# Performance work log

Hardware: AMD Instinct MI355X
Metric: run time of the kernel (lower is better)

Reference implementation:

```python
import jax, jax.numpy as jnp
import numpy as np

EPS_GN = 1e-5
EPS_ATTN = 1e-6
HEADS = 4
DIM_HEAD = 32
GROUPS = 32  # min(32, channels=128)


def group_norm(x, weight, bias, groups=GROUPS, eps=EPS_GN):
    # x: [b, c, h, w]
    b, c, h, w = x.shape
    xg = x.reshape(b, groups, c // groups, h, w)
    mean = xg.mean(axis=(2, 3, 4), keepdims=True)
    var = xg.var(axis=(2, 3, 4), keepdims=True)
    xg = (xg - mean) * jax.lax.rsqrt(var + eps)
    x = xg.reshape(b, c, h, w)
    return x * weight[None, :, None, None] + bias[None, :, None, None]


def conv1x1(x, w):
    # x: [b, c, h, w], w: [out, in] -> [b, out, h, w]
    return jnp.einsum('bchw,oc->bohw', x, w)


def setup_inputs() -> dict:
    key = jax.random.key(0)
    ks = jax.random.split(key, 6)
    b, c, h, w = 16, 128, 128, 128
    inner = HEADS * DIM_HEAD  # 128
    x = jax.random.normal(ks[0], (b, c, h, w), dtype=jnp.float32)
    gn1_w = jnp.ones((c,), jnp.float32) + 0.02 * jax.random.normal(ks[1], (c,), jnp.float32)
    gn1_b = 0.02 * jax.random.normal(ks[2], (c,), jnp.float32)
    w_qkv = jax.random.normal(ks[3], (inner * 3, c), jnp.float32) / np.sqrt(c)
    w_out = jax.random.normal(ks[4], (c, inner), jnp.float32) / np.sqrt(inner)
    gn2_w = jnp.ones((c,), jnp.float32) + 0.02 * jax.random.normal(ks[5], (c,), jnp.float32)
    gn2_b = jnp.zeros((c,), jnp.float32)
    return {"x": x, "gn1_w": gn1_w, "gn1_b": gn1_b, "w_qkv": w_qkv,
            "w_out": w_out, "gn2_w": gn2_w, "gn2_b": gn2_b}


def reference(x, gn1_w, gn1_b, w_qkv, w_out, gn2_w, gn2_b):
    b, c, h, w = x.shape
    residual = x
    xn = group_norm(x, gn1_w, gn1_b)
    qkv = conv1x1(xn, w_qkv)                      # [b, 3*inner, h, w]
    q, k, v = jnp.split(qkv, 3, axis=1)
    # 'b (heads d) h w -> b heads (h w) d'
    def to_tokens(t):
        return t.reshape(b, HEADS, DIM_HEAD, h * w).transpose(0, 1, 3, 2)
    q, k, v = to_tokens(q), to_tokens(k), to_tokens(v)
    q = jax.nn.elu(q) + 1.0
    k = jax.nn.elu(k) + 1.0
    k_sum = k.sum(axis=2)                          # [b, heads, d]
    kv = jnp.einsum('bhnd,bhne->bhde', k, v)       # [b, heads, d, d]
    qk_sum = jnp.einsum('bhnd,bhd->bhn', q, k_sum) # [b, heads, n]
    qkv_out = jnp.einsum('bhnd,bhde->bhne', q, kv) # [b, heads, n, d]
    out = qkv_out / (qk_sum[..., None] + EPS_ATTN)
    # 'b heads (h w) d -> b (heads d) h w'
    out = out.transpose(0, 1, 3, 2).reshape(b, HEADS * DIM_HEAD, h, w)
    out = conv1x1(out, w_out)
    out = group_norm(out, gn2_w, gn2_b)
    return out + residual
```

## Files before the change

kernel.cpp:

```cpp
#include <hip/hip_runtime.h>

#define B_   16
#define C_   128
#define HW_  16384

typedef __attribute__((ext_vector_type(4))) float  floatx4;
typedef __attribute__((ext_vector_type(8))) short  short8;
typedef __attribute__((ext_vector_type(4))) short  short4v;

static __device__ __forceinline__ unsigned short f2bf(float f){
  unsigned int u = __float_as_uint(f);
  u += 0x7FFFu + ((u >> 16) & 1u);
  return (unsigned short)(u >> 16);
}
static __device__ __forceinline__ float bf2f(unsigned short h){
  return __uint_as_float(((unsigned int)h) << 16);
}
static __device__ __forceinline__ float elu1(float v){
  return v > 0.f ? v + 1.f : __expf(v);
}
static __device__ __forceinline__ int keyx(int n){ return ((n >> 1) & 7) ^ ((n >> 4) & 7); }

__global__ __launch_bounds__(512) void k_xprep(const float* __restrict__ x,
    unsigned short* __restrict__ xT, float* __restrict__ gn1part){
  int blk = blockIdx.x;
  int b = blk >> 6, tile = blk & 63;
  int n0 = tile * 256;
  __shared__ unsigned short XS[32768];
  int t = threadIdx.x, w = t >> 6, l = t & 63;
  float sk[4], sk2[4];
  #pragma unroll
  for (int k = 0; k < 4; ++k){ sk[k] = 0.f; sk2[k] = 0.f; }
  #pragma unroll
  for (int k = 0; k < 4; ++k){
    float4 f4[4];
    #pragma unroll
    for (int j = 0; j < 4; ++j){
      int c = 16*w + 4*k + j;
      f4[j] = *(const float4*)(x + ((size_t)(b*128 + c))*HW_ + n0 + 4*l);
    }
    #pragma unroll
    for (int j = 0; j < 4; ++j){
      sk[k]  += f4[j].x + f4[j].y + f4[j].z + f4[j].w;
      sk2[k] += f4[j].x*f4[j].x + f4[j].y*f4[j].y + f4[j].z*f4[j].z + f4[j].w*f4[j].w;
    }
    int c0 = 16*w + 4*k, cs = c0 >> 3, co = c0 & 7;
    #pragma unroll
    for (int i = 0; i < 4; ++i){
      int n = 4*l + i;
      short4v p;
      #pragma unroll
      for (int j = 0; j < 4; ++j) p[j] = (short)f2bf(((const float*)&f4[j])[i]);
      *(short4v*)(XS + n*128 + (((cs ^ keyx(n)) << 3) + co)) = p;
    }
  }
  #pragma unroll
  for (int k = 0; k < 4; ++k){
    float a = sk[k], q = sk2[k];
    #pragma unroll
    for (int o = 32; o; o >>= 1){ a += __shfl_down(a, o); q += __shfl_down(q, o); }
    if (l == 0){
      gn1part[((size_t)blk)*64 + (4*w + k)*2 + 0] = a;
      gn1part[((size_t)blk)*64 + (4*w + k)*2 + 1] = q;
    }
  }
  __syncthreads();
  unsigned short* dst = xT + ((size_t)blk)*32768;
  for (int it = 0; it < 8; ++it){
    int slot = t + it*512;
    *(short8*)(dst + slot*8) = *(const short8*)(XS + slot*8);
  }
}

__global__ __launch_bounds__(64) void k_gn1fin(const float* __restrict__ gn1part,
    float* __restrict__ mean, float* __restrict__ rstd){
  int bg = blockIdx.x;
  int b = bg >> 5, g = bg & 31, l = threadIdx.x;
  const float* p = gn1part + ((size_t)(b*64 + l))*64 + g*2;
  float s = p[0], s2 = p[1];
  #pragma unroll
  for (int o = 32; o; o >>= 1){ s += __shfl_down(s, o); s2 += __shfl_down(s2, o); }
  if (l == 0){
    float m = s * (1.f/65536.f);
    float var = s2 * (1.f/65536.f) - m*m;
    mean[bg] = m; rstd[bg] = rsqrtf(var + 1e-5f);
  }
}

__global__ __launch_bounds__(64) void k_fold(const float* __restrict__ wqkv, const float* __restrict__ wout,
    const float* __restrict__ g1w, const float* __restrict__ g1b,
    const float* __restrict__ mean, const float* __restrict__ rstd,
    unsigned short* __restrict__ wqp, float* __restrict__ bias, unsigned short* __restrict__ woutb){
  int i = blockIdx.x, l = threadIdx.x;
  if (i < 6144){
    int b = i / 384, o = i % 384;
    float bsum = 0.f;
    #pragma unroll
    for (int j = 0; j < 2; ++j){
      int c = l*2 + j, g = c >> 2;
      float m = mean[b*32 + g], r = rstd[b*32 + g];
      float A  = r * g1w[c];
      float Bc = g1b[c] - m * A;
      float wv = wqkv[o*128 + c];
      wqp[((size_t)(b*384 + o))*128 + c] = f2bf(wv * A);
      bsum += wv * Bc;
    }
    #pragma unroll
    for (int o2 = 32; o2; o2 >>= 1) bsum += __shfl_down(bsum, o2);
    if (l == 0) bias[b*384 + o] = bsum;
  } else {
    int r = i - 6144;
    #pragma unroll
    for (int j = 0; j < 2; ++j){ int c = l*2 + j; woutb[r*128 + c] = f2bf(wout[r*128 + c]); }
  }
}

__global__ __launch_bounds__(512) void k_kv(const unsigned short* __restrict__ xT,
    const unsigned short* __restrict__ wqp, const float* __restrict__ bias,
    float* __restrict__ kvpart, float* __restrict__ ksumpart){
  int blk = blockIdx.x;
  int b = blk >> 6;
  __shared__ unsigned short S[32768];
  int t = threadIdx.x, w = t >> 6, lane = t & 63, lr = lane & 15, lk = lane >> 4;
  short8 wfr[2][4]; float biasv[2];
  #pragma unroll
  for (int rt = 0; rt < 2; ++rt){
    int o = 128 + rt*128 + w*16;
    #pragma unroll
    for (int ks = 0; ks < 4; ++ks)
      wfr[rt][ks] = *(const short8*)(wqp + ((size_t)(b*384 + o + lr))*128 + ks*32 + lk*8);
    biasv[rt] = bias[b*384 + o + lr];
  }
  short8 ones;
  #pragma unroll
  for (int j = 0; j < 8; ++j) ones[j] = (short)0x3F80;
  floatx4 accA = {0,0,0,0}, accB = {0,0,0,0}, ksaA = {0,0,0,0}, ksaB = {0,0,0,0};
  for (int half = 0; half < 2; ++half){
    const unsigned short* src = xT + ((size_t)blk)*32768 + half*16384;
    for (int it = 0; it < 4; ++it){
      int slot = t + it*512;
      *(short8*)(S + slot*8) = *(const short8*)(src + slot*8);
    }
    __syncthreads();
    short4v kpk[8], vpk[8];
    for (int ct = 0; ct < 8; ++ct){
      int nr = ct*16 + lr;
      int kn = keyx(nr);
      short8 xfr[4];
      #pragma unroll
      for (int ks = 0; ks < 4; ++ks)
        xfr[ks] = *(const short8*)(S + nr*128 + (((ks*4 + lk) ^ kn) << 3));
      #pragma unroll
      for (int rt = 0; rt < 2; ++rt){
        floatx4 acc = {0.f,0.f,0.f,0.f};
        #pragma unroll
        for (int ks = 0; ks < 4; ++ks)
          acc = __builtin_amdgcn_mfma_f32_16x16x32_bf16(xfr[ks], wfr[rt][ks], acc, 0,0,0);
        short4v pk;
        #pragma unroll
        for (int r = 0; r < 4; ++r){
          float v = acc[r] + biasv[rt];
          if (rt == 0) v = elu1(v);
          pk[r] = (short)f2bf(v);
        }
        if (rt == 0) kpk[ct] = pk; else vpk[ct] = pk;
      }
    }
    __syncthreads();
    #pragma unroll
    for (int ct = 0; ct < 8; ++ct){
      int cimg = w*16 + lr;
      int n0 = ct*16 + lk*4;
      int off = cimg*128 + ((((n0 >> 3) ^ ((cimg >> 1) & 7)) << 3) + (n0 & 7));
      *(short4v*)(S + off)         = kpk[ct];
      *(short4v*)(S + 16384 + off) = vpk[ct];
    }
    __syncthreads();
    #pragma unroll
    for (int j = 0; j < 2; ++j){
      int m = w + 8*j;
      int h = m >> 2, dt = (m >> 1) & 1, et = m & 1;
      int arow = h*32 + dt*16 + lr, brow = h*32 + et*16 + lr;
      int akey = (lr >> 1) & 7;
      #pragma unroll
      for (int ks = 0; ks < 4; ++ks){
        short8 ka = *(const short8*)(S + arow*128 + (((ks*4 + lk) ^ akey) << 3));
        short8 vb = *(const short8*)(S + 16384 + brow*128 + (((ks*4 + lk) ^ akey) << 3));
        if (j == 0){
          accA = __builtin_amdgcn_mfma_f32_16x16x32_bf16(ka, vb, accA, 0,0,0);
          if (et == 0) ksaA = __builtin_amdgcn_mfma_f32_16x16x32_bf16(ka, ones, ksaA, 0,0,0);
        } else {
          accB = __builtin_amdgcn_mfma_f32_16x16x32_bf16(ka, vb, accB, 0,0,0);
          if (et == 0) ksaB = __builtin_amdgcn_mfma_f32_16x16x32_bf16(ka, ones, ksaB, 0,0,0);
        }
      }
    }
    __syncthreads();
  }
  #pragma unroll
  for (int j = 0; j < 2; ++j){
    int m = w + 8*j;
    int h = m >> 2, dt = (m >> 1) & 1, et = m & 1;
    floatx4 acc = j ? accB : accA, ksa = j ? ksaB : ksaA;
    float* kvp = kvpart + ((size_t)(blk*4 + h))*1024;
    #pragma unroll
    for (int r = 0; r < 4; ++r)
      kvp[(dt*16 + lk*4 + r)*32 + et*16 + lr] = acc[r];
    if (et == 0 && lr == 0){
      float* ksp = ksumpart + ((size_t)(blk*4 + h))*32;
      #pragma unroll
      for (int r = 0; r < 4; ++r) ksp[dt*16 + lk*4 + r] = ksa[r];
    }
  }
}

__global__ __launch_bounds__(256) void k_kvmfold(const float* __restrict__ kvpart, const float* __restrict__ ksumpart,
    const unsigned short* __restrict__ woutb, unsigned short* __restrict__ Mb, float* __restrict__ ksumF){
  int bh = blockIdx.x, t = threadIdx.x;
  int b = bh >> 2, h = bh & 3;
  __shared__ float kvL[1024];
  for (int i = t; i < 1024; i += 256){
    float s = 0.f;
    for (int nt = 0; nt < 64; ++nt) s += kvpart[((size_t)((b*64 + nt)*4 + h))*1024 + i];
    kvL[i] = s;
  }
  if (t < 32){
    float s = 0.f;
    for (int nt = 0; nt < 64; ++nt) s += ksumpart[((size_t)((b*64 + nt)*4 + h))*32 + t];
    ksumF[b*128 + h*32 + t] = s;
  }
  __syncthreads();
  int o = t >> 1, d0 = (t & 1)*16;
  float w2row[32];
  #pragma unroll
  for (int e = 0; e < 32; ++e) w2row[e] = bf2f(woutb[o*128 + h*32 + e]);
  for (int dd = 0; dd < 16; ++dd){
    int d = d0 + dd;
    float s = 0.f;
    #pragma unroll
    for (int e = 0; e < 32; ++e) s += w2row[e] * kvL[d*32 + e];
    Mb[((size_t)b)*16384 + o*128 + h*32 + d] = f2bf(s);
  }
}

__global__ __launch_bounds__(512) void k_attn2(const unsigned short* __restrict__ xT,
    const unsigned short* __restrict__ wqp, const float* __restrict__ bias,
    const float* __restrict__ ksumF, const unsigned short* __restrict__ Mb,
    unsigned short* __restrict__ hbT, float* __restrict__ gn2part){
  int blk = blockIdx.x;
  int b = blk >> 6;
  __shared__ unsigned short S[32768];
  int t = threadIdx.x, w = t >> 6, lane = t & 63, lr = lane & 15, lk = lane >> 4;
  int rg = w & 3, cg = w >> 2;
  const unsigned short* src = xT + ((size_t)blk)*32768;
  for (int it = 0; it < 8; ++it){
    int slot = t + it*512;
    *(short8*)(S + slot*8) = *(const short8*)(src + slot*8);
  }
  short8 afr[2][4]; float biasq[2][4], ksL[2][4];
  #pragma unroll
  for (int rtl = 0; rtl < 2; ++rtl){
    int o = rg*32 + rtl*16;
    #pragma unroll
    for (int ks = 0; ks < 4; ++ks)
      afr[rtl][ks] = *(const short8*)(wqp + ((size_t)(b*384 + o + lr))*128 + ks*32 + lk*8);
    #pragma unroll
    for (int r = 0; r < 4; ++r){
      biasq[rtl][r] = bias[b*384 + o + lk*4 + r];
      ksL[rtl][r]   = ksumF[b*128 + o + lk*4 + r];
    }
  }
  __syncthreads();
  short4v qpk[2][8];
  for (int ct = 0; ct < 8; ++ct){
    int nr = cg*128 + ct*16 + lr;
    int kn = keyx(nr);
    short8 bfr[4];
    #pragma unroll
    for (int ks = 0; ks < 4; ++ks)
      bfr[ks] = *(const short8*)(S + nr*128 + (((ks*4 + lk) ^ kn) << 3));
    float qv[2][4];
    #pragma unroll
    for (int rtl = 0; rtl < 2; ++rtl){
      floatx4 acc = {0.f,0.f,0.f,0.f};
      #pragma unroll
      for (int ks = 0; ks < 4; ++ks)
        acc = __builtin_amdgcn_mfma_f32_16x16x32_bf16(afr[rtl][ks], bfr[ks], acc, 0,0,0);
      #pragma unroll
      for (int r = 0; r < 4; ++r) qv[rtl][r] = elu1(acc[r] + biasq[rtl][r]);
    }
    float p = 0.f;
    #pragma unroll
    for (int rtl = 0; rtl < 2; ++rtl)
      #pragma unroll
      for (int r = 0; r < 4; ++r) p += ksL[rtl][r] * qv[rtl][r];
    p += __shfl_xor(p, 16);
    p += __shfl_xor(p, 32);
    float inv = 1.f / (p + 1e-6f);
    #pragma unroll
    for (int rtl = 0; rtl < 2; ++rtl){
      short4v pk;
      #pragma unroll
      for (int r = 0; r < 4; ++r) pk[r] = (short)f2bf(qv[rtl][r] * inv);
      qpk[rtl][ct] = pk;
    }
  }
  short8 afr2[2][4];
  #pragma unroll
  for (int rtl = 0; rtl < 2; ++rtl)
    #pragma unroll
    for (int ks = 0; ks < 4; ++ks)
      afr2[rtl][ks] = *(const short8*)(Mb + ((size_t)b)*16384 + (size_t)((rg*2 + rtl)*16 + lr)*128 + ks*32 + lk*8);
  __syncthreads();
  #pragma unroll
  for (int rtl = 0; rtl < 2; ++rtl){
    int c0 = rg*32 + rtl*16 + lk*4;
    #pragma unroll
    for (int ct = 0; ct < 8; ++ct){
      int n = cg*128 + ct*16 + lr;
      *(short4v*)(S + n*128 + ((((c0 >> 3) ^ (n & 7)) << 3) + (c0 & 7))) = qpk[rtl][ct];
    }
  }
  __syncthreads();
  unsigned short* hdst = hbT + ((size_t)blk)*32768;
  float gs[2][4], gq[2][4];
  #pragma unroll
  for (int rtl = 0; rtl < 2; ++rtl)
    #pragma unroll
    for (int r = 0; r < 4; ++r){ gs[rtl][r] = 0.f; gq[rtl][r] = 0.f; }
  for (int ct = 0; ct < 8; ++ct){
    int nr = cg*128 + ct*16 + lr;
    short8 bfr[4];
    #pragma unroll
    for (int ks = 0; ks < 4; ++ks)
      bfr[ks] = *(const short8*)(S + nr*128 + (((ks*4 + lk) ^ (nr & 7)) << 3));
    #pragma unroll
    for (int rtl = 0; rtl < 2; ++rtl){
      floatx4 acc = {0.f,0.f,0.f,0.f};
      #pragma unroll
      for (int ks = 0; ks < 4; ++ks)
        acc = __builtin_amdgcn_mfma_f32_16x16x32_bf16(afr2[rtl][ks], bfr[ks], acc, 0,0,0);
      short4v pk;
      #pragma unroll
      for (int r = 0; r < 4; ++r){
        float hv = acc[r];
        pk[r] = (short)f2bf(hv);
        gs[rtl][r] += hv; gq[rtl][r] += hv*hv;
      }
      *(short4v*)(hdst + (((rg*2 + rtl)*16 + cg*8 + ct)*256 + lane*4)) = pk;
    }
  }
  #pragma unroll
  for (int m = 1; m < 16; m <<= 1)
    #pragma unroll
    for (int rtl = 0; rtl < 2; ++rtl)
      #pragma unroll
      for (int r = 0; r < 4; ++r){ gs[rtl][r] += __shfl_xor(gs[rtl][r], m); gq[rtl][r] += __shfl_xor(gq[rtl][r], m); }
  if (lr == 0){
    #pragma unroll
    for (int rtl = 0; rtl < 2; ++rtl)
      #pragma unroll
      for (int r = 0; r < 4; ++r){
        int c = (rg*2 + rtl)*16 + lk*4 + r;
        gn2part[((size_t)(blk*2 + cg)*128 + c)*2 + 0] = gs[rtl][r];
        gn2part[((size_t)(blk*2 + cg)*128 + c)*2 + 1] = gq[rtl][r];
      }
  }
}

__global__ __launch_bounds__(64) void k_gn2stats(const float* __restrict__ gn2part,
    float* __restrict__ mean, float* __restrict__ rstd){
  int b = blockIdx.x >> 5, g = blockIdx.x & 31;
  int lane = threadIdx.x;
  float s = 0.f, s2 = 0.f;
  #pragma unroll
  for (int cgi = 0; cgi < 2; ++cgi)
    #pragma unroll
    for (int j = 0; j < 4; ++j){
      const float* p = gn2part + ((size_t)(((b*64 + lane)*2 + cgi)*128 + g*4 + j))*2;
      s += p[0]; s2 += p[1];
    }
  #pragma unroll
  for (int o = 32; o; o >>= 1){ s += __shfl_down(s, o); s2 += __shfl_down(s2, o); }
  if (lane == 0){
    float m = s * (1.f/65536.f);
    float var = s2 * (1.f/65536.f) - m*m;
    mean[blockIdx.x] = m; rstd[blockIdx.x] = rsqrtf(var + 1e-5f);
  }
}

__global__ __launch_bounds__(256) void k_final(const unsigned short* __restrict__ hbT,
    const unsigned short* __restrict__ xT, float* __restrict__ out,
    const float* __restrict__ mean, const float* __restrict__ rstd,
    const float* __restrict__ g2w, const float* __restrict__ g2b){
  int blk = blockIdx.x;
  int b = blk >> 7, t128 = blk & 127;
  int tile = t128 >> 1, half = t128 & 1;
  __shared__ unsigned short HS[16384];
  __shared__ unsigned short XS[16384];
  int t = threadIdx.x;
  const unsigned short* hsrc = hbT + ((size_t)(b*64 + tile))*32768;
  const unsigned short* xsrc = xT + ((size_t)(b*64 + tile))*32768 + half*16384;
  for (int it = 0; it < 8; ++it){
    int slot = t + it*256;
    int w8 = slot >> 8, rest = slot & 255;
    *(short8*)(HS + slot*8) = *(const short8*)(hsrc + ((w8*16 + half*8)*256 + rest*8));
    *(short8*)(XS + slot*8) = *(const short8*)(xsrc + slot*8);
  }
  __syncthreads();
  for (int it = 0; it < 8; ++it){
    int idx = t + it*256;
    int c = idx >> 4, oct = idx & 15;
    int bg = b*32 + (c >> 2);
    float m = mean[bg], r = rstd[bg];
    float sc = r * g2w[c], sh = g2b[c] - m * sc;
    int hbase0 = ((c >> 4)*8 + (oct >> 1))*256 + ((c >> 2) & 3)*64 + (oct & 1)*32 + (c & 3);
    float ov[8];
    #pragma unroll
    for (int j = 0; j < 8; ++j){
      int n = oct*8 + j;
      float hv = bf2f(HS[hbase0 + j*4]);
      unsigned short xv = XS[n*128 + ((((c >> 3) ^ keyx(n)) << 3) + (c & 7))];
      ov[j] = hv*sc + sh + bf2f(xv);
    }
    float* op = out + ((size_t)(b*128 + c))*HW_ + t128*128 + oct*8;
    float4 o0, o1;
    o0.x = ov[0]; o0.y = ov[1]; o0.z = ov[2]; o0.w = ov[3];
    o1.x = ov[4]; o1.y = ov[5]; o1.z = ov[6]; o1.w = ov[7];
    *(float4*)op = o0; *(float4*)(op + 4) = o1;
  }
}

extern "C" void kernel_launch(void* const* d_in, const int* in_sizes, int n_in,
                              void* d_out, int out_size, void* d_ws, size_t ws_size,
                              hipStream_t stream){
  const float* x    = (const float*)d_in[0];
  const float* g1w  = (const float*)d_in[1];
  const float* g1b  = (const float*)d_in[2];
  const float* wqkv = (const float*)d_in[3];
  const float* wout = (const float*)d_in[4];
  const float* g2w  = (const float*)d_in[5];
  const float* g2b  = (const float*)d_in[6];
  char* ws = (char*)d_ws;
  (void)in_sizes; (void)n_in; (void)out_size; (void)ws_size;

  float* gn1part  = (float*)(ws + 0);
  float* gn1_mean = (float*)(ws + 262144);
  float* gn1_rstd = (float*)(ws + 264192);
  float* gn2_mean = (float*)(ws + 266240);
  float* gn2_rstd = (float*)(ws + 268288);
  float* bias     = (float*)(ws + 270336);
  unsigned short* woutb = (unsigned short*)(ws + 294912);
  float* ksumF    = (float*)(ws + 327680);
  unsigned short* Mb = (unsigned short*)(ws + 335872);
  unsigned short* wqp = (unsigned short*)(ws + 860160);
  float* ksumpart = (float*)(ws + 2433024);
  float* kvpart   = (float*)(ws + 4194304);
  float* gn2part  = (float*)(ws + 37748736);
  unsigned short* xT  = (unsigned short*)(ws + 46137344);
  unsigned short* hbT = (unsigned short*)(ws + 113246208);

  k_xprep<<<dim3(1024), dim3(512), 0, stream>>>(x, xT, gn1part);
  k_gn1fin<<<dim3(512), dim3(64), 0, stream>>>(gn1part, gn1_mean, gn1_rstd);
  k_fold<<<dim3(6272), dim3(64), 0, stream>>>(wqkv, wout, g1w, g1b, gn1_mean, gn1_rstd, wqp, bias, woutb);
  k_kv<<<dim3(1024), dim3(512), 0, stream>>>(xT, wqp, bias, kvpart, ksumpart);
  k_kvmfold<<<dim3(64), dim3(256), 0, stream>>>(kvpart, ksumpart, woutb, Mb, ksumF);
  k_attn2<<<dim3(1024), dim3(512), 0, stream>>>(xT, wqp, bias, ksumF, Mb, hbT, gn2part);
  k_gn2stats<<<dim3(512), dim3(64), 0, stream>>>(gn2part, gn2_mean, gn2_rstd);
  k_final<<<dim3(2048), dim3(256), 0, stream>>>(hbT, xT, (float*)d_out, gn2_mean, gn2_rstd, g2w, g2b);
}
```

Measured before the change: 220.8 us.

## Halve k_attn2 token tile to 128 and raise occupancy with launch bounds

Result: slower. 237.3 us (+7.5%).

```diff
diff --git a/kernel.cpp b/kernel.cpp
--- a/kernel.cpp
+++ b/kernel.cpp
@@ -243,17 +243,17 @@
   }
 }
 
-__global__ __launch_bounds__(512) void k_attn2(const unsigned short* __restrict__ xT,
+__global__ __launch_bounds__(512, 6) void k_attn2(const unsigned short* __restrict__ xT,
     const unsigned short* __restrict__ wqp, const float* __restrict__ bias,
     const float* __restrict__ ksumF, const unsigned short* __restrict__ Mb,
     unsigned short* __restrict__ hbT, float* __restrict__ gn2part){
   int blk = blockIdx.x;
-  int b = blk >> 6;
-  __shared__ unsigned short S[32768];
+  int b = blk >> 7, t128 = blk & 127;
+  __shared__ unsigned short S[16384];
   int t = threadIdx.x, w = t >> 6, lane = t & 63, lr = lane & 15, lk = lane >> 4;
   int rg = w & 3, cg = w >> 2;
-  const unsigned short* src = xT + ((size_t)blk)*32768;
-  for (int it = 0; it < 8; ++it){
+  const unsigned short* src = xT + ((size_t)(b*64 + (t128 >> 1)))*32768 + (t128 & 1)*16384;
+  for (int it = 0; it < 4; ++it){
     int slot = t + it*512;
     *(short8*)(S + slot*8) = *(const short8*)(src + slot*8);
   }
@@ -271,9 +271,10 @@
     }
   }
   __syncthreads();
-  short4v qpk[2][8];
-  for (int ct = 0; ct < 8; ++ct){
-    int nr = cg*128 + ct*16 + lr;
+  short4v qpk[2][4];
+  #pragma unroll
+  for (int ct = 0; ct < 4; ++ct){
+    int nr = cg*64 + ct*16 + lr;
     int kn = keyx(nr);
     short8 bfr[4];
     #pragma unroll
@@ -305,66 +306,54 @@
       qpk[rtl][ct] = pk;
     }
   }
-  short8 afr2[2][4];
-  #pragma unroll
-  for (int rtl = 0; rtl < 2; ++rtl)
-    #pragma unroll
-    for (int ks = 0; ks < 4; ++ks)
-      afr2[rtl][ks] = *(const short8*)(Mb + ((size_t)b)*16384 + (size_t)((rg*2 + rtl)*16 + lr)*128 + ks*32 + lk*8);
+  short8 afr2[4];
+  #pragma unroll
+  for (int ks = 0; ks < 4; ++ks)
+    afr2[ks] = *(const short8*)(Mb + ((size_t)b)*16384 + (size_t)(w*16 + lr)*128 + ks*32 + lk*8);
   __syncthreads();
   #pragma unroll
   for (int rtl = 0; rtl < 2; ++rtl){
     int c0 = rg*32 + rtl*16 + lk*4;
     #pragma unroll
-    for (int ct = 0; ct < 8; ++ct){
-      int n = cg*128 + ct*16 + lr;
+    for (int ct = 0; ct < 4; ++ct){
+      int n = cg*64 + ct*16 + lr;
       *(short4v*)(S + n*128 + ((((c0 >> 3) ^ (n & 7)) << 3) + (c0 & 7))) = qpk[rtl][ct];
     }
   }
   __syncthreads();
-  unsigned short* hdst = hbT + ((size_t)blk)*32768;
-  float gs[2][4], gq[2][4];
-  #pragma unroll
-  for (int rtl = 0; rtl < 2; ++rtl)
-    #pragma unroll
-    for (int r = 0; r < 4; ++r){ gs[rtl][r] = 0.f; gq[rtl][r] = 0.f; }
+  unsigned short* hdst = hbT + ((size_t)blk)*16384;
+  float gs[4] = {0,0,0,0}, gq[4] = {0,0,0,0};
+  #pragma unroll
   for (int ct = 0; ct < 8; ++ct){
-    int nr = cg*128 + ct*16 + lr;
+    int nr = ct*16 + lr;
     short8 bfr[4];
     #pragma unroll
     for (int ks = 0; ks < 4; ++ks)
       bfr[ks] = *(const short8*)(S + nr*128 + (((ks*4 + lk) ^ (nr & 7)) << 3));
-    #pragma unroll
-    for (int rtl = 0; rtl < 2; ++rtl){
-      floatx4 acc = {0.f,0.f,0.f,0.f};
-      #pragma unroll
-      for (int ks = 0; ks < 4; ++ks)
-        acc = __builtin_amdgcn_mfma_f32_16x16x32_bf16(afr2[rtl][ks], bfr[ks], acc, 0,0,0);
-      short4v pk;
-      #pragma unroll
-      for (int r = 0; r < 4; ++r){
-        float hv = acc[r];
-        pk[r] = (short)f2bf(hv);
-        gs[rtl][r] += hv; gq[rtl][r] += hv*hv;
-      }
-      *(short4v*)(hdst + (((rg*2 + rtl)*16 + cg*8 + ct)*256 + lane*4)) = pk;
-    }
+    floatx4 acc = {0.f,0.f,0.f,0.f};
+    #pragma unroll
+    for (int ks = 0; ks < 4; ++ks)
+      acc = __builtin_amdgcn_mfma_f32_16x16x32_bf16(afr2[ks], bfr[ks], acc, 0,0,0);
+    short4v pk;
+    #pragma unroll
+    for (int r = 0; r < 4; ++r){
+      float hv = acc[r];
+      pk[r] = (short)f2bf(hv);
+      gs[r] += hv; gq[r] += hv*hv;
+    }
+    *(short4v*)(hdst + (w*8 + ct)*256 + lane*4) = pk;
   }
   #pragma unroll
   for (int m = 1; m < 16; m <<= 1)
     #pragma unroll
-    for (int rtl = 0; rtl < 2; ++rtl)
-      #pragma unroll
-      for (int r = 0; r < 4; ++r){ gs[rtl][r] += __shfl_xor(gs[rtl][r], m); gq[rtl][r] += __shfl_xor(gq[rtl][r], m); }
+    for (int r = 0; r < 4; ++r){ gs[r] += __shfl_xor(gs[r], m); gq[r] += __shfl_xor(gq[r], m); }
   if (lr == 0){
     #pragma unroll
-    for (int rtl = 0; rtl < 2; ++rtl)
-      #pragma unroll
-      for (int r = 0; r < 4; ++r){
-        int c = (rg*2 + rtl)*16 + lk*4 + r;
-        gn2part[((size_t)(blk*2 + cg)*128 + c)*2 + 0] = gs[rtl][r];
-        gn2part[((size_t)(blk*2 + cg)*128 + c)*2 + 1] = gq[rtl][r];
-      }
+    for (int r = 0; r < 4; ++r){
+      int c = w*16 + lk*4 + r;
+      gn2part[((size_t)blk*128 + c)*2 + 0] = gs[r];
+      gn2part[((size_t)blk*128 + c)*2 + 1] = gq[r];
+    }
   }
 }
 
@@ -374,12 +363,12 @@
   int lane = threadIdx.x;
   float s = 0.f, s2 = 0.f;
   #pragma unroll
-  for (int cgi = 0; cgi < 2; ++cgi)
-    #pragma unroll
-    for (int j = 0; j < 4; ++j){
-      const float* p = gn2part + ((size_t)(((b*64 + lane)*2 + cgi)*128 + g*4 + j))*2;
-      s += p[0]; s2 += p[1];
-    }
+  for (int rr = 0; rr < 2; ++rr){
+    int row = lane + rr*64;
+    const float* p = gn2part + ((size_t)(b*128 + row))*256 + g*8;
+    #pragma unroll
+    for (int j = 0; j < 4; ++j){ s += p[j*2]; s2 += p[j*2 + 1]; }
+  }
   #pragma unroll
   for (int o = 32; o; o >>= 1){ s += __shfl_down(s, o); s2 += __shfl_down(s2, o); }
   if (lane == 0){
@@ -395,16 +384,14 @@
     const float* __restrict__ g2w, const float* __restrict__ g2b){
   int blk = blockIdx.x;
   int b = blk >> 7, t128 = blk & 127;
-  int tile = t128 >> 1, half = t128 & 1;
   __shared__ unsigned short HS[16384];
   __shared__ unsigned short XS[16384];
   int t = threadIdx.x;
-  const unsigned short* hsrc = hbT + ((size_t)(b*64 + tile))*32768;
-  const unsigned short* xsrc = xT + ((size_t)(b*64 + tile))*32768 + half*16384;
+  const unsigned short* hsrc = hbT + ((size_t)blk)*16384;
+  const unsigned short* xsrc = xT + ((size_t)(b*64 + (t128 >> 1)))*32768 + (t128 & 1)*16384;
   for (int it = 0; it < 8; ++it){
     int slot = t + it*256;
-    int w8 = slot >> 8, rest = slot & 255;
-    *(short8*)(HS + slot*8) = *(const short8*)(hsrc + ((w8*16 + half*8)*256 + rest*8));
+    *(short8*)(HS + slot*8) = *(const short8*)(hsrc + slot*8);
     *(short8*)(XS + slot*8) = *(const short8*)(xsrc + slot*8);
   }
   __syncthreads();
@@ -465,7 +452,7 @@
   k_fold<<<dim3(6272), dim3(64), 0, stream>>>(wqkv, wout, g1w, g1b, gn1_mean, gn1_rstd, wqp, bias, woutb);
   k_kv<<<dim3(1024), dim3(512), 0, stream>>>(xT, wqp, bias, kvpart, ksumpart);
   k_kvmfold<<<dim3(64), dim3(256), 0, stream>>>(kvpart, ksumpart, woutb, Mb, ksumF);
-  k_attn2<<<dim3(1024), dim3(512), 0, stream>>>(xT, wqp, bias, ksumF, Mb, hbT, gn2part);
+  k_attn2<<<dim3(2048), dim3(512), 0, stream>>>(xT, wqp, bias, ksumF, Mb, hbT, gn2part);
   k_gn2stats<<<dim3(512), dim3(64), 0, stream>>>(gn2part, gn2_mean, gn2_rstd);
   k_final<<<dim3(2048), dim3(256), 0, stream>>>(hbT, xT, (float*)d_out, gn2_mean, gn2_rstd, g2w, g2b);
 }
```
